# Performance work log

Hardware: AMD Instinct MI355X
Metric: run time of the kernel (lower is better)

The kernel has to match this reference:

```python
import jax, jax.numpy as jnp
import numpy as np

B, F, N, NO = 1, 512, 8192, 21
L1, L2, L3 = 640, 256, 128


def setup_inputs() -> dict:
    key = jax.random.key(0)
    ks = jax.random.split(key, 32)
    rn = lambda k, s: jax.random.normal(k, s, dtype=jnp.float32)
    inp = {
        "emb1": rn(ks[0], (B, F, N)),
        "emb2": rn(ks[1], (B, F, N)),
        "t1": rn(ks[2], (B, 3, N)),
        "t2": rn(ks[3], (B, 3, N)),
        "obj": jax.random.randint(ks[4], (B, 1), 0, NO, dtype=jnp.int32),
    }
    # 1x1 Conv1d weights == dense (out,in) matrices + bias
    dims_r = [(L1, 2 * F), (L2, L1), (L3, L2), (NO * 4, L3)]
    dims_t = [(L1, 2 * F), (L2, L1), (L3, L2), (NO * 3, L3)]
    ki = 5
    for br, dims in (("r", dims_r), ("t", dims_t)):
        for i, (o, c) in enumerate(dims, start=1):
            inp[f"w{i}{br}"] = rn(ks[ki], (o, c)) * (1.0 / np.sqrt(c)); ki += 1
            inp[f"b{i}{br}"] = rn(ks[ki], (o,)) * 0.01; ki += 1
    return inp


def _knn1(ref, qry):
    # ref, qry: (3, N). For each query point j, index of nearest ref point.
    g = ref.T @ qry  # (N_ref, N_qry)
    d2 = jnp.sum(ref * ref, axis=0)[:, None] + jnp.sum(qry * qry, axis=0)[None, :] - 2.0 * g
    return jnp.argmin(d2, axis=0)  # (N_qry,)


def _branch(x, w1, b1, w2, b2, w3, b3, w4, b4):
    h = jax.nn.relu(w1 @ x + b1[:, None])
    h = jax.nn.relu(w2 @ h + b2[:, None])
    h = jax.nn.relu(w3 @ h + b3[:, None])
    return w4 @ h + b4[:, None]


def reference(emb1, emb2, t1, t2, obj,
              w1r, b1r, w2r, b2r, w3r, b3r, w4r, b4r,
              w1t, b1t, w2t, b2t, w3t, b3t, w4t, b4t):
    bs, num_feat, num_points = emb1.shape
    t1 = t1.reshape(bs, 3, -1)
    t2 = t2.reshape(bs, 3, -1)
    # brute-force 1-NN of each t2 point among t1 points (bs == 1)
    idx = _knn1(t1[0], t2[0])  # (N,) zero-based (torch code subtracts 1 from 1-based inds)
    emb1g = emb1[0][:, idx]  # gather matched features, (F, N)
    # torch.stack([emb1,emb2],dim=1).view(bs, 2F, N) == channel concat [emb1g; emb2]
    emb = jnp.concatenate([emb1g, emb2[0]], axis=0)  # (2F, N)
    rx = _branch(emb, w1r, b1r, w2r, b2r, w3r, b3r, w4r, b4r).reshape(NO, 4, num_points)
    tx = _branch(emb, w1t, b1t, w2t, b2t, w3t, b3t, w4t, b4t).reshape(NO, 3, num_points)
    obj0 = obj[0]  # (1,)
    out_rx = jnp.transpose(rx[obj0], (0, 2, 1))  # (1, N, 4)
    out_tx = jnp.transpose(tx[obj0], (0, 2, 1))  # (1, N, 3)
    return out_rx, out_tx
```

## Files before the change

### kernel.cpp

```cpp
#include <hip/hip_runtime.h>

typedef unsigned short u16;
typedef __bf16 bf16x8 __attribute__((ext_vector_type(8)));
typedef float f32x4 __attribute__((ext_vector_type(4)));

__device__ __forceinline__ float b2f(u16 v) {
    return __uint_as_float(((unsigned int)v) << 16);
}
__device__ __forceinline__ u16 f2b(float f) {
    unsigned int u = __float_as_uint(f);
    u += 0x7fffu + ((u >> 16) & 1u);
    return (u16)(u >> 16);
}
__device__ __forceinline__ unsigned int pk2(float a, float b) {
    return (unsigned int)f2b(a) | ((unsigned int)f2b(b) << 16);
}

__global__ void knn_k(const float* __restrict__ t1, const float* __restrict__ t2,
                      unsigned long long* __restrict__ keys)
{
    __shared__ float4 ref[128];
    const int t = threadIdx.x;
    const int rs = blockIdx.x;
    const int qb = blockIdx.y;
    if (t < 128) {
        int i = rs * 128 + t;
        float x = t1[i], y = t1[8192 + i], z = t1[16384 + i];
        float rr = __fadd_rn(__fadd_rn(__fmul_rn(x, x), __fmul_rn(y, y)), __fmul_rn(z, z));
        ref[t] = make_float4(x, y, z, rr);
    }
    __syncthreads();

    float qx[8], qy[8], qz[8], qq[8], bestd[8];
    int besti[8];
    const int q0 = qb * 2048 + t;
#pragma unroll
    for (int j = 0; j < 8; ++j) {
        int q = q0 + j * 256;
        qx[j] = t2[q]; qy[j] = t2[8192 + q]; qz[j] = t2[16384 + q];
        qq[j] = __fadd_rn(__fadd_rn(__fmul_rn(qx[j], qx[j]), __fmul_rn(qy[j], qy[j])),
                          __fmul_rn(qz[j], qz[j]));
        bestd[j] = __uint_as_float(0x7f800000u);
        besti[j] = 0;
    }
    for (int i = 0; i < 128; ++i) {
        float4 r = ref[i];
        int ridx = rs * 128 + i;
#pragma unroll
        for (int j = 0; j < 8; ++j) {
            float g = __fmaf_rn(qz[j], r.z, __fmaf_rn(qy[j], r.y, __fmul_rn(qx[j], r.x)));
            float d2 = __fsub_rn(__fadd_rn(r.w, qq[j]), __fmul_rn(2.0f, g));
            if (d2 < bestd[j]) { bestd[j] = d2; besti[j] = ridx; }
        }
    }
#pragma unroll
    for (int j = 0; j < 8; ++j) {
        unsigned long long key =
            ((unsigned long long)__float_as_uint(bestd[j]) << 32) | (unsigned int)besti[j];
        atomicMin(&keys[q0 + j * 256], key);
    }
}

__global__ void transpose_k(const float* __restrict__ in, u16* __restrict__ out,
                            int ostride, int coff)
{
    __shared__ float tile[64][66];
    const int t = threadIdx.x;
    const int n0 = blockIdx.x * 64, f0 = blockIdx.y * 64;
    const int c = t & 63, r4 = t >> 6;
#pragma unroll
    for (int p = 0; p < 16; ++p) {
        int fr = p * 4 + r4;
        tile[fr][c] = in[(size_t)(f0 + fr) * 8192 + n0 + c];
    }
    __syncthreads();
#pragma unroll
    for (int p = 0; p < 16; ++p) {
        int nr = p * 4 + r4;
        out[(size_t)(n0 + nr) * ostride + coff + f0 + c] = f2b(tile[c][nr]);
    }
}

__global__ void gather_k(const unsigned long long* __restrict__ keys,
                         const u16* __restrict__ emb1t, u16* __restrict__ Xt)
{
    const int t = threadIdx.x, w = t >> 6, l = t & 63;
    const int nbase = blockIdx.x * 32;
#pragma unroll
    for (int it = 0; it < 8; ++it) {
        int n = nbase + it * 4 + w;
        int i = (int)(keys[n] & 0xffffffffu);
        const uint4* src = (const uint4*)(emb1t + (size_t)i * 512);
        uint4* dst = (uint4*)(Xt + (size_t)n * 1024);
        dst[l] = src[l];
    }
}

__global__ __launch_bounds__(256, 3) void gemm_bt(
    const float* __restrict__ Ar, const float* __restrict__ At,
    const float* __restrict__ biasr, const float* __restrict__ biast,
    const u16* __restrict__ Bt, u16* __restrict__ Ct,
    int Mh, int K, int bstride, int b_step, int ostride, int relu)
{
    __shared__ __align__(16) u16 lds_a[128 * 32];
    __shared__ __align__(16) u16 lds_b[128 * 32];

    const int t = threadIdx.x;
    const int n0 = blockIdx.x * 128;
    const int m0 = blockIdx.y * 128;
    const int branch = blockIdx.z;

    const float* A = branch ? At : Ar;
    const float* bias = branch ? biast : biasr;
    const int b_off = branch * b_step;
    const int out_off = branch * Mh;

    const int srow = t >> 2;
    const int schunk = t & 3;
    const int sslot = (schunk ^ ((srow >> 1) & 3)) * 8;
    const float* ga0 = A + (size_t)(m0 + srow) * K + schunk * 8;
    const float* ga1 = ga0 + (size_t)64 * K;
    const u16* gb0 = Bt + (size_t)(n0 + srow) * bstride + b_off + schunk * 8;
    const u16* gb1 = gb0 + (size_t)64 * bstride;
    u16* la0 = &lds_a[srow * 32 + sslot];
    u16* la1 = la0 + 64 * 32;
    u16* lb0 = &lds_b[srow * 32 + sslot];
    u16* lb1 = lb0 + 64 * 32;

    const int w = t >> 6, l = t & 63;
    const int wm = (w & 1) << 6, wn = (w >> 1) << 6;
    const int lrow = l & 15, quad = l >> 4;
    const int rslot = (quad ^ ((lrow >> 1) & 3)) * 8;
    const u16* fa = &lds_a[(wm + lrow) * 32 + rslot];
    const u16* fb = &lds_b[(wn + lrow) * 32 + rslot];

    f32x4 acc[4][4];
#pragma unroll
    for (int i = 0; i < 4; ++i)
#pragma unroll
        for (int j = 0; j < 4; ++j)
            acc[i][j] = (f32x4){0.f, 0.f, 0.f, 0.f};

    float4 a0l = *(const float4*)ga0, a0h = *(const float4*)(ga0 + 4);
    float4 a1l = *(const float4*)ga1, a1h = *(const float4*)(ga1 + 4);
    uint4 b0 = *(const uint4*)gb0, b1 = *(const uint4*)gb1;

    for (int kt = 0; kt < K; kt += 32) {
        __syncthreads();
        uint4 wa0, wa1;
        wa0.x = pk2(a0l.x, a0l.y); wa0.y = pk2(a0l.z, a0l.w);
        wa0.z = pk2(a0h.x, a0h.y); wa0.w = pk2(a0h.z, a0h.w);
        wa1.x = pk2(a1l.x, a1l.y); wa1.y = pk2(a1l.z, a1l.w);
        wa1.z = pk2(a1h.x, a1h.y); wa1.w = pk2(a1h.z, a1h.w);
        *(uint4*)la0 = wa0; *(uint4*)la1 = wa1;
        *(uint4*)lb0 = b0;  *(uint4*)lb1 = b1;
        __syncthreads();
        if (kt + 32 < K) {
            ga0 += 32; ga1 += 32; gb0 += 32; gb1 += 32;
            a0l = *(const float4*)ga0; a0h = *(const float4*)(ga0 + 4);
            a1l = *(const float4*)ga1; a1h = *(const float4*)(ga1 + 4);
            b0 = *(const uint4*)gb0;   b1 = *(const uint4*)gb1;
        }
        bf16x8 af[4], bfr[4];
#pragma unroll
        for (int i = 0; i < 4; ++i) {
            af[i]  = *(const bf16x8*)(fa + i * 16 * 32);
            bfr[i] = *(const bf16x8*)(fb + i * 16 * 32);
        }
#pragma unroll
        for (int i = 0; i < 4; ++i)
#pragma unroll
            for (int j = 0; j < 4; ++j)
                acc[i][j] = __builtin_amdgcn_mfma_f32_16x16x32_bf16(
                    af[i], bfr[j], acc[i][j], 0, 0, 0);
    }

#pragma unroll
    for (int i = 0; i < 4; ++i) {
        const int mbase = m0 + wm + i * 16 + quad * 4;
        const float4 bbv = *(const float4*)&bias[mbase];
#pragma unroll
        for (int j = 0; j < 4; ++j) {
            const int n = n0 + wn + j * 16 + lrow;
            f32x4 v = acc[i][j];
            float x0 = v[0] + bbv.x, x1 = v[1] + bbv.y;
            float x2 = v[2] + bbv.z, x3 = v[3] + bbv.w;
            if (relu) {
                x0 = fmaxf(x0, 0.f); x1 = fmaxf(x1, 0.f);
                x2 = fmaxf(x2, 0.f); x3 = fmaxf(x3, 0.f);
            }
            ushort4 o;
            o.x = f2b(x0); o.y = f2b(x1); o.z = f2b(x2); o.w = f2b(x3);
            *(ushort4*)&Ct[(size_t)n * ostride + out_off + mbase] = o;
        }
    }
}

__global__ void final_k(const u16* __restrict__ h3t,
                        const float* __restrict__ w4r, const float* __restrict__ b4r,
                        const float* __restrict__ w4t, const float* __restrict__ b4t,
                        const int* __restrict__ objp, float* __restrict__ out)
{
    __shared__ float wr[4 * 128], wt[3 * 128], bb[7];
    const int t = threadIdx.x;
    const int o = objp[0];
    if (t < 128) {
#pragma unroll
        for (int r = 0; r < 4; ++r) wr[r * 128 + t] = w4r[(o * 4 + r) * 128 + t];
#pragma unroll
        for (int r = 0; r < 3; ++r) wt[r * 128 + t] = w4t[(o * 3 + r) * 128 + t];
    } else if (t < 135) {
        int r = t - 128;
        bb[r] = (r < 4) ? b4r[o * 4 + r] : b4t[o * 3 + (r - 4)];
    }
    __syncthreads();

    const int n = blockIdx.x * 256 + t;
    const u16* hp = h3t + (size_t)n * 256;
    float ar0 = 0, ar1 = 0, ar2 = 0, ar3 = 0, at0 = 0, at1 = 0, at2 = 0;
#pragma unroll
    for (int k = 0; k < 128; k += 8) {
        uint4 hv = *(const uint4*)(hp + k);
        const u16* hs = (const u16*)&hv;
        uint4 gv = *(const uint4*)(hp + 128 + k);
        const u16* gs = (const u16*)&gv;
#pragma unroll
        for (int j = 0; j < 8; ++j) {
            float h = b2f(hs[j]);
            ar0 = fmaf(h, wr[k + j], ar0);
            ar1 = fmaf(h, wr[128 + k + j], ar1);
            ar2 = fmaf(h, wr[256 + k + j], ar2);
            ar3 = fmaf(h, wr[384 + k + j], ar3);
            float g = b2f(gs[j]);
            at0 = fmaf(g, wt[k + j], at0);
            at1 = fmaf(g, wt[128 + k + j], at1);
            at2 = fmaf(g, wt[256 + k + j], at2);
        }
    }
    float4 ro = make_float4(ar0 + bb[0], ar1 + bb[1], ar2 + bb[2], ar3 + bb[3]);
    *(float4*)&out[n * 4] = ro;
    float* tp = out + 32768 + n * 3;
    tp[0] = at0 + bb[4]; tp[1] = at1 + bb[5]; tp[2] = at2 + bb[6];
}

extern "C" void kernel_launch(void* const* d_in, const int* in_sizes, int n_in,
                              void* d_out, int out_size, void* d_ws, size_t ws_size,
                              hipStream_t stream)
{
    const float* emb1 = (const float*)d_in[0];
    const float* emb2 = (const float*)d_in[1];
    const float* t1   = (const float*)d_in[2];
    const float* t2   = (const float*)d_in[3];
    const int*   obj  = (const int*)d_in[4];
    const float* w1r = (const float*)d_in[5];  const float* b1r = (const float*)d_in[6];
    const float* w2r = (const float*)d_in[7];  const float* b2r = (const float*)d_in[8];
    const float* w3r = (const float*)d_in[9];  const float* b3r = (const float*)d_in[10];
    const float* w4r = (const float*)d_in[11]; const float* b4r = (const float*)d_in[12];
    const float* w1t = (const float*)d_in[13]; const float* b1t = (const float*)d_in[14];
    const float* w2t = (const float*)d_in[15]; const float* b2t = (const float*)d_in[16];
    const float* w3t = (const float*)d_in[17]; const float* b3t = (const float*)d_in[18];
    const float* w4t = (const float*)d_in[19]; const float* b4t = (const float*)d_in[20];

    char* ws = (char*)d_ws;
    unsigned long long* keys = (unsigned long long*)ws;
    u16* emb1t = (u16*)(ws + (1u << 16));
    u16* Xt    = (u16*)(ws + (1u << 16) + (8u << 20));
    u16* h1t   = (u16*)(ws + (1u << 16) + (24u << 20));
    u16* h2t   = emb1t;
    u16* h3t   = Xt;

    hipMemsetAsync(keys, 0xFF, 8192 * sizeof(unsigned long long), stream);
    knn_k<<<dim3(64, 4), 256, 0, stream>>>(t1, t2, keys);
    transpose_k<<<dim3(128, 8), 256, 0, stream>>>(emb1, emb1t, 512, 0);
    transpose_k<<<dim3(128, 8), 256, 0, stream>>>(emb2, Xt, 1024, 512);
    gather_k<<<256, 256, 0, stream>>>(keys, emb1t, Xt);
    gemm_bt<<<dim3(64, 5, 2), 256, 0, stream>>>(w1r, w1t, b1r, b1t, Xt,  h1t, 640, 1024, 1024,   0, 1280, 1);
    gemm_bt<<<dim3(64, 2, 2), 256, 0, stream>>>(w2r, w2t, b2r, b2t, h1t, h2t, 256,  640, 1280, 640,  512, 1);
    gemm_bt<<<dim3(64, 1, 2), 256, 0, stream>>>(w3r, w3t, b3r, b3t, h2t, h3t, 128,  256,  512, 256,  256, 1);
    final_k<<<32, 256, 0, stream>>>(h3t, w4r, b4r, w4t, b4t, obj, (float*)d_out);
}
```

Before: 224.6 us.

## Pre-pack weights to bf16 and stream GEMM tiles via direct global-to-LDS loads

A new kernel converts the layer 1-3 weights to bf16 once per call, so the GEMMs no longer convert fp32 weights tile by tile. The GEMM now fills LDS with global_load_lds (16-byte direct-to-LDS loads) issued right after fragments are read, which drops the register staging and the XOR swizzle. It is templated on N-tile width so layers 2-3 use 64-wide tiles and launch twice as many blocks. The two transposes are merged into one launch. The costs are an extra launch plus a weight pass each call, and possible LDS bank conflicts now that the swizzle is gone.

```diff
diff --git a/kernel.cpp b/kernel.cpp
--- a/kernel.cpp
+++ b/kernel.cpp
@@ -12,8 +12,33 @@
     u += 0x7fffu + ((u >> 16) & 1u);
     return (u16)(u >> 16);
 }
-__device__ __forceinline__ unsigned int pk2(float a, float b) {
-    return (unsigned int)f2b(a) | ((unsigned int)f2b(b) << 16);
+
+__device__ __forceinline__ void ld_lds16(const u16* g, u16* l) {
+    __builtin_amdgcn_global_load_lds(
+        (__attribute__((address_space(1))) void*)(uintptr_t)(const void*)g,
+        (__attribute__((address_space(3))) void*)l, 16, 0, 0);
+}
+
+__global__ void pack_w_k(const float* __restrict__ w1r, const float* __restrict__ w1t,
+                         const float* __restrict__ w2r, const float* __restrict__ w2t,
+                         const float* __restrict__ w3r, const float* __restrict__ w3t,
+                         u16* __restrict__ dst)
+{
+    size_t i = (size_t)blockIdx.x * 2048 + (size_t)threadIdx.x * 8;
+    const float* src; size_t off;
+    if (i < 655360)       { src = w1r; off = 0; }
+    else if (i < 1310720) { src = w1t; off = 655360; }
+    else if (i < 1474560) { src = w2r; off = 1310720; }
+    else if (i < 1638400) { src = w2t; off = 1474560; }
+    else if (i < 1671168) { src = w3r; off = 1638400; }
+    else                  { src = w3t; off = 1671168; }
+    const float4 lo = *(const float4*)(src + (i - off));
+    const float4 hi = *(const float4*)(src + (i - off) + 4);
+    ushort4 o0, o1;
+    o0.x = f2b(lo.x); o0.y = f2b(lo.y); o0.z = f2b(lo.z); o0.w = f2b(lo.w);
+    o1.x = f2b(hi.x); o1.y = f2b(hi.y); o1.z = f2b(hi.z); o1.w = f2b(hi.w);
+    *(ushort4*)(dst + i) = o0;
+    *(ushort4*)(dst + i + 4) = o1;
 }
 
 __global__ void knn_k(const float* __restrict__ t1, const float* __restrict__ t2,
@@ -61,10 +86,14 @@
     }
 }
 
-__global__ void transpose_k(const float* __restrict__ in, u16* __restrict__ out,
-                            int ostride, int coff)
+__global__ void transpose_k(const float* __restrict__ e1, const float* __restrict__ e2,
+                            u16* __restrict__ o1, u16* __restrict__ o2)
 {
     __shared__ float tile[64][66];
+    const float* in = blockIdx.z ? e2 : e1;
+    u16* out = blockIdx.z ? o2 : o1;
+    const int ostride = blockIdx.z ? 1024 : 512;
+    const int coff = blockIdx.z ? 512 : 0;
     const int t = threadIdx.x;
     const int n0 = blockIdx.x * 64, f0 = blockIdx.y * 64;
     const int c = t & 63, r4 = t >> 6;
@@ -96,81 +125,83 @@
     }
 }
 
-__global__ __launch_bounds__(256, 3) void gemm_bt(
-    const float* __restrict__ Ar, const float* __restrict__ At,
+template <int TN>
+__global__ __launch_bounds__(256) void gemm_bt(
+    const u16* __restrict__ Ar, const u16* __restrict__ At,
     const float* __restrict__ biasr, const float* __restrict__ biast,
     const u16* __restrict__ Bt, u16* __restrict__ Ct,
     int Mh, int K, int bstride, int b_step, int ostride, int relu)
 {
+    constexpr int NJ = TN / 32;
     __shared__ __align__(16) u16 lds_a[128 * 32];
-    __shared__ __align__(16) u16 lds_b[128 * 32];
+    __shared__ __align__(16) u16 lds_b[TN * 32];
 
     const int t = threadIdx.x;
-    const int n0 = blockIdx.x * 128;
+    const int n0 = blockIdx.x * TN;
     const int m0 = blockIdx.y * 128;
     const int branch = blockIdx.z;
 
-    const float* A = branch ? At : Ar;
+    const u16* A = branch ? At : Ar;
     const float* bias = branch ? biast : biasr;
     const int b_off = branch * b_step;
     const int out_off = branch * Mh;
 
-    const int srow = t >> 2;
-    const int schunk = t & 3;
-    const int sslot = (schunk ^ ((srow >> 1) & 3)) * 8;
-    const float* ga0 = A + (size_t)(m0 + srow) * K + schunk * 8;
-    const float* ga1 = ga0 + (size_t)64 * K;
-    const u16* gb0 = Bt + (size_t)(n0 + srow) * bstride + b_off + schunk * 8;
-    const u16* gb1 = gb0 + (size_t)64 * bstride;
-    u16* la0 = &lds_a[srow * 32 + sslot];
-    u16* la1 = la0 + 64 * 32;
-    u16* lb0 = &lds_b[srow * 32 + sslot];
-    u16* lb1 = lb0 + 64 * 32;
-
     const int w = t >> 6, l = t & 63;
-    const int wm = (w & 1) << 6, wn = (w >> 1) << 6;
+    const int sr = l >> 2, sc = (l & 3) * 8;
+
+    const u16* gA0 = A + (size_t)(m0 + w * 32 + sr) * K + sc;
+    const u16* gA1 = gA0 + (size_t)16 * K;
+    u16* lA0 = &lds_a[w * 1024];
+    u16* lA1 = lA0 + 512;
+
+    const u16* gB0;
+    const u16* gB1 = nullptr;
+    u16 *lB0, *lB1 = nullptr;
+    if (TN == 128) {
+        gB0 = Bt + (size_t)(n0 + w * 32 + sr) * bstride + b_off + sc;
+        gB1 = gB0 + (size_t)16 * bstride;
+        lB0 = &lds_b[w * 1024];
+        lB1 = lB0 + 512;
+    } else {
+        gB0 = Bt + (size_t)(n0 + w * 16 + sr) * bstride + b_off + sc;
+        lB0 = &lds_b[w * 512];
+    }
+
+    const int wm = (w & 1) * 64;
+    const int wn = (w >> 1) * (TN / 2);
     const int lrow = l & 15, quad = l >> 4;
-    const int rslot = (quad ^ ((lrow >> 1) & 3)) * 8;
-    const u16* fa = &lds_a[(wm + lrow) * 32 + rslot];
-    const u16* fb = &lds_b[(wn + lrow) * 32 + rslot];
-
-    f32x4 acc[4][4];
+    const u16* fa = &lds_a[(wm + lrow) * 32 + quad * 8];
+    const u16* fb = &lds_b[(wn + lrow) * 32 + quad * 8];
+
+    f32x4 acc[4][NJ];
 #pragma unroll
     for (int i = 0; i < 4; ++i)
 #pragma unroll
-        for (int j = 0; j < 4; ++j)
+        for (int j = 0; j < NJ; ++j)
             acc[i][j] = (f32x4){0.f, 0.f, 0.f, 0.f};
 
-    float4 a0l = *(const float4*)ga0, a0h = *(const float4*)(ga0 + 4);
-    float4 a1l = *(const float4*)ga1, a1h = *(const float4*)(ga1 + 4);
-    uint4 b0 = *(const uint4*)gb0, b1 = *(const uint4*)gb1;
+    ld_lds16(gA0, lA0); ld_lds16(gA1, lA1);
+    ld_lds16(gB0, lB0);
+    if (TN == 128) ld_lds16(gB1, lB1);
 
     for (int kt = 0; kt < K; kt += 32) {
         __syncthreads();
-        uint4 wa0, wa1;
-        wa0.x = pk2(a0l.x, a0l.y); wa0.y = pk2(a0l.z, a0l.w);
-        wa0.z = pk2(a0h.x, a0h.y); wa0.w = pk2(a0h.z, a0h.w);
-        wa1.x = pk2(a1l.x, a1l.y); wa1.y = pk2(a1l.z, a1l.w);
-        wa1.z = pk2(a1h.x, a1h.y); wa1.w = pk2(a1h.z, a1h.w);
-        *(uint4*)la0 = wa0; *(uint4*)la1 = wa1;
-        *(uint4*)lb0 = b0;  *(uint4*)lb1 = b1;
+        bf16x8 af[4], bfr[NJ];
+#pragma unroll
+        for (int i = 0; i < 4; ++i) af[i] = *(const bf16x8*)(fa + i * 16 * 32);
+#pragma unroll
+        for (int j = 0; j < NJ; ++j) bfr[j] = *(const bf16x8*)(fb + j * 16 * 32);
         __syncthreads();
         if (kt + 32 < K) {
-            ga0 += 32; ga1 += 32; gb0 += 32; gb1 += 32;
-            a0l = *(const float4*)ga0; a0h = *(const float4*)(ga0 + 4);
-            a1l = *(const float4*)ga1; a1h = *(const float4*)(ga1 + 4);
-            b0 = *(const uint4*)gb0;   b1 = *(const uint4*)gb1;
+            gA0 += 32; gA1 += 32; gB0 += 32;
+            ld_lds16(gA0, lA0); ld_lds16(gA1, lA1);
+            ld_lds16(gB0, lB0);
+            if (TN == 128) { gB1 += 32; ld_lds16(gB1, lB1); }
         }
-        bf16x8 af[4], bfr[4];
-#pragma unroll
-        for (int i = 0; i < 4; ++i) {
-            af[i]  = *(const bf16x8*)(fa + i * 16 * 32);
-            bfr[i] = *(const bf16x8*)(fb + i * 16 * 32);
-        }
 #pragma unroll
         for (int i = 0; i < 4; ++i)
 #pragma unroll
-            for (int j = 0; j < 4; ++j)
+            for (int j = 0; j < NJ; ++j)
                 acc[i][j] = __builtin_amdgcn_mfma_f32_16x16x32_bf16(
                     af[i], bfr[j], acc[i][j], 0, 0, 0);
     }
@@ -180,7 +211,7 @@
         const int mbase = m0 + wm + i * 16 + quad * 4;
         const float4 bbv = *(const float4*)&bias[mbase];
 #pragma unroll
-        for (int j = 0; j < 4; ++j) {
+        for (int j = 0; j < NJ; ++j) {
             const int n = n0 + wn + j * 16 + lrow;
             f32x4 v = acc[i][j];
             float x0 = v[0] + bbv.x, x1 = v[1] + bbv.y;
@@ -266,16 +297,21 @@
     u16* emb1t = (u16*)(ws + (1u << 16));
     u16* Xt    = (u16*)(ws + (1u << 16) + (8u << 20));
     u16* h1t   = (u16*)(ws + (1u << 16) + (24u << 20));
+    u16* wp    = (u16*)(ws + (1u << 16) + (44u << 20));
     u16* h2t   = emb1t;
     u16* h3t   = Xt;
 
+    u16* w1rp = wp;            u16* w1tp = wp + 655360;
+    u16* w2rp = wp + 1310720;  u16* w2tp = wp + 1474560;
+    u16* w3rp = wp + 1638400;  u16* w3tp = wp + 1671168;
+
     hipMemsetAsync(keys, 0xFF, 8192 * sizeof(unsigned long long), stream);
+    pack_w_k<<<832, 256, 0, stream>>>(w1r, w1t, w2r, w2t, w3r, w3t, wp);
     knn_k<<<dim3(64, 4), 256, 0, stream>>>(t1, t2, keys);
-    transpose_k<<<dim3(128, 8), 256, 0, stream>>>(emb1, emb1t, 512, 0);
-    transpose_k<<<dim3(128, 8), 256, 0, stream>>>(emb2, Xt, 1024, 512);
+    transpose_k<<<dim3(128, 8, 2), 256, 0, stream>>>(emb1, emb2, emb1t, Xt);
     gather_k<<<256, 256, 0, stream>>>(keys, emb1t, Xt);
-    gemm_bt<<<dim3(64, 5, 2), 256, 0, stream>>>(w1r, w1t, b1r, b1t, Xt,  h1t, 640, 1024, 1024,   0, 1280, 1);
-    gemm_bt<<<dim3(64, 2, 2), 256, 0, stream>>>(w2r, w2t, b2r, b2t, h1t, h2t, 256,  640, 1280, 640,  512, 1);
-    gemm_bt<<<dim3(64, 1, 2), 256, 0, stream>>>(w3r, w3t, b3r, b3t, h2t, h3t, 128,  256,  512, 256,  256, 1);
+    gemm_bt<128><<<dim3(64, 5, 2), 256, 0, stream>>>(w1rp, w1tp, b1r, b1t, Xt,  h1t, 640, 1024, 1024,   0, 1280, 1);
+    gemm_bt<64><<<dim3(128, 2, 2), 256, 0, stream>>>(w2rp, w2tp, b2r, b2t, h1t, h2t, 256,  640, 1280, 640,  512, 1);
+    gemm_bt<64><<<dim3(128, 1, 2), 256, 0, stream>>>(w3rp, w3tp, b3r, b3t, h2t, h3t, 128,  256,  512, 256,  256, 1);
     final_k<<<32, 256, 0, stream>>>(h3t, w4r, b4r, w4t, b4t, obj, (float*)d_out);
 }
```

After: 210.5 us. 1.07x faster.
